# Performance work log

Measured on AMD Instinct MI355X. Metric: run time of the kernel, lower is better.

Reference implementation:

```python
import jax, jax.numpy as jnp
import numpy as np

B, SQ, SK = 2, 2048, 2048
D_MODEL, N_HEADS = 1024, 16
D_HEAD = D_MODEL // N_HEADS
LN_EPS = 1e-5


def _ln(x, w, b):
    # per-head LayerNorm over last dim (d_head)
    mu = jnp.mean(x, axis=-1, keepdims=True)
    var = jnp.mean(jnp.square(x - mu), axis=-1, keepdims=True)
    return (x - mu) * jax.lax.rsqrt(var + LN_EPS) * w + b


def setup_inputs() -> dict:
    key = jax.random.key(0)
    ks = jax.random.split(key, 8)
    sd = 1.0 / np.sqrt(D_MODEL)
    so = 1.0 / np.sqrt(D_HEAD)
    return {
        "x_q": jax.random.normal(ks[0], (B, SQ, D_MODEL), jnp.float32),
        "x_kv": jax.random.normal(ks[1], (B, SK, D_MODEL), jnp.float32),
        "mask": jnp.tril(jnp.ones((SQ, SK), dtype=bool)),  # causal
        "W_Q": jax.random.normal(ks[2], (N_HEADS, D_MODEL, D_HEAD), jnp.float32) * sd,
        "W_K": jax.random.normal(ks[3], (N_HEADS, D_MODEL, D_HEAD), jnp.float32) * sd,
        "W_V": jax.random.normal(ks[4], (N_HEADS, D_MODEL, D_HEAD), jnp.float32) * sd,
        "W_O": jax.random.normal(ks[5], (N_HEADS, D_HEAD, D_MODEL), jnp.float32) * so,
        "b_Q": jnp.zeros((N_HEADS, D_HEAD), jnp.float32),
        "b_K": jnp.zeros((N_HEADS, D_HEAD), jnp.float32),
        "b_V": jnp.zeros((N_HEADS, D_HEAD), jnp.float32),
        "b_O": jnp.zeros((D_MODEL,), jnp.float32),
        "ln1_w": jnp.ones((D_HEAD,), jnp.float32),
        "ln1_b": jnp.zeros((D_HEAD,), jnp.float32),
        "ln2_w": jnp.ones((D_HEAD,), jnp.float32),
        "ln2_b": jnp.zeros((D_HEAD,), jnp.float32),
    }


def reference(x_q, x_kv, mask, W_Q, W_K, W_V, W_O, b_Q, b_K, b_V, b_O,
              ln1_w, ln1_b, ln2_w, ln2_b):
    # QKV projections: b s d, n d h -> b s n h
    q = jnp.einsum('bsd,ndh->bsnh', x_q, W_Q) + b_Q
    k = jnp.einsum('bsd,ndh->bsnh', x_kv, W_K) + b_K
    v = jnp.einsum('bsd,ndh->bsnh', x_kv, W_V) + b_V
    # QK-norm (ln_first=False, rope=None -> just apply LN after projections)
    q = _ln(q, ln1_w, ln1_b)
    k = _ln(k, ln2_w, ln2_b)
    # NOTE: no 1/sqrt(d_head) scaling, matching the original module
    att = jnp.einsum('bqnh,bknh->bnqk', q, k)
    att = jnp.where(mask, att, -jnp.inf)
    probas = jax.nn.softmax(att, axis=-1)
    z = jnp.einsum('bnqk,bknh->bqnh', probas, v)
    out = jnp.einsum('bqnh,nhd->bqd', z, W_O) + b_O
    return (out, k, v)
```

## Files before the change

### kernel.cpp

```cpp
#include <hip/hip_runtime.h>
#include <hip/hip_bf16.h>

#define B_   2
#define SQ_  2048
#define DM_  1024
#define NH_  16
#define DH_  64

typedef __attribute__((ext_vector_type(8))) short          bf16x8;
typedef __attribute__((ext_vector_type(4))) short          bf16x4;
typedef __attribute__((ext_vector_type(8))) unsigned short u16x8;
typedef __attribute__((ext_vector_type(4))) float          f32x4;

__device__ __forceinline__ unsigned short f2bf(float f) {
    union { __hip_bfloat16 h; unsigned short u; } c;
    c.h = __float2bfloat16(f);
    return c.u;
}
__device__ __forceinline__ float gsum16(float v) {
    v += __shfl_xor(v, 1);
    v += __shfl_xor(v, 2);
    v += __shfl_xor(v, 4);
    v += __shfl_xor(v, 8);
    return v;
}

__device__ __forceinline__ f32x4 mfma16(bf16x4 a, bf16x4 b, f32x4 c) {
#if __has_builtin(__builtin_amdgcn_mfma_f32_16x16x16bf16_1k)
    return __builtin_amdgcn_mfma_f32_16x16x16bf16_1k(a, b, c, 0, 0, 0);
#else
    asm("v_mfma_f32_16x16x16_bf16 %0, %1, %2, %0" : "+v"(c) : "v"(a), "v"(b));
    return c;
#endif
}

__device__ __forceinline__ void gll16(const unsigned short* g, unsigned short* l) {
    __builtin_amdgcn_global_load_lds(
        (const __attribute__((address_space(1))) unsigned int*)g,
        (__attribute__((address_space(3))) unsigned int*)l,
        16, 0, 0);
}

__global__ __launch_bounds__(256) void prep_all(
    const float* __restrict__ W_Q, const float* __restrict__ W_K,
    const float* __restrict__ W_V, const float* __restrict__ W_O,
    const float* __restrict__ x_q, const float* __restrict__ x_kv,
    unsigned short* __restrict__ WTq, unsigned short* __restrict__ WTkv,
    unsigned short* __restrict__ WTo,
    unsigned short* __restrict__ xqbf, unsigned short* __restrict__ xkvbf)
{
    const int bid = blockIdx.x, tid = threadIdx.x;
    if (bid >= 1024) {
        const int cid = bid - 1024;
        const float* src = (cid < 512) ? x_q : x_kv;
        unsigned short* dst = (cid < 512) ? xqbf : xkvbf;
        const size_t base = (size_t)(cid & 511) * 8192 + tid * 4;
#pragma unroll
        for (int i = 0; i < 8; ++i) {
            const float4 v = *(const float4*)(src + base + i * 1024);
            ushort4 o;
            o.x = f2bf(v.x); o.y = f2bf(v.y); o.z = f2bf(v.z); o.w = f2bf(v.w);
            *(ushort4*)(dst + base + i * 1024) = o;
        }
        return;
    }
    __shared__ float t[64][65];
    const float* src; unsigned short* dst; int R, C, r0, c0;
    if (bid < 768) {
        const int which = bid >> 8, rem = bid & 255;
        const int rblk = rem & 15, zz = rem >> 4;
        src = (which == 0) ? W_Q : (which == 1) ? W_K : W_V;
        dst = (which == 0) ? WTq : (which == 1) ? WTkv : (WTkv + (1u << 20));
        src += (size_t)65536 * zz;
        dst += (size_t)65536 * zz;
        R = 1024; C = 64; r0 = rblk * 64; c0 = 0;
    } else {
        const int rem = bid - 768;
        src = W_O; dst = WTo; R = 1024; C = 1024;
        r0 = (rem & 15) * 64; c0 = (rem >> 4) * 64;
    }
    const int lr = tid >> 6, lc = tid & 63;
#pragma unroll
    for (int i = 0; i < 16; ++i)
        t[lr + i * 4][lc] = src[(size_t)(r0 + lr + i * 4) * C + c0 + lc];
    __syncthreads();
    const int u = tid & 15, w0 = tid >> 4;
#pragma unroll
    for (int i = 0; i < 4; ++i) {
        const int cl = w0 + i * 16;
        ushort4 o;
        o.x = f2bf(t[4 * u + 0][cl]);
        o.y = f2bf(t[4 * u + 1][cl]);
        o.z = f2bf(t[4 * u + 2][cl]);
        o.w = f2bf(t[4 * u + 3][cl]);
        *(ushort4*)&dst[(size_t)(c0 + cl) * R + r0 + 4 * u] = o;
    }
}

template <int TM, int MODE>
__device__ __forceinline__ void gemm_body(
    unsigned short (*__restrict__ As)[64], unsigned short (*__restrict__ Bs)[64],
    int bx, int by, const unsigned short* __restrict__ Abf,
    const unsigned short* __restrict__ WT,
    const float* __restrict__ biasK, const float* __restrict__ biasV,
    const float* __restrict__ lnw, const float* __restrict__ lnb,
    float* __restrict__ Cf, float* __restrict__ Cf2,
    unsigned short* __restrict__ Cb, unsigned short* __restrict__ CbT, int tid)
{
    constexpr int MI = (TM >= 32) ? TM / 32 : 1;
    constexpr int AJ = TM / 32;

    const int m0 = by * TM;
    const int c0 = bx * 128;

    const int wid = tid >> 6, lane = tid & 63;
    const int wm = (wid >> 1) * (TM / 2);
    const int wn = (wid & 1) * 64;
    const int l15 = lane & 15, qd = lane >> 4;

    const int srow  = tid >> 3;
    const int pslot = tid & 7;
    const int sslot = pslot ^ (srow & 7);
    const unsigned short* Ag = Abf + (size_t)(m0 + (srow % TM)) * 1024 + sslot * 8;
    const unsigned short* Bg = WT  + (size_t)(c0 + srow) * 1024 + sslot * 8;
    unsigned short* Al = &As[srow % TM][pslot * 8];
    unsigned short* Bl = &Bs[srow][pslot * 8];
    const bool athr = (srow < TM);

    const f32x4 zero4 = {0.f, 0.f, 0.f, 0.f};
    f32x4 acc[MI][4];
#pragma unroll
    for (int mi = 0; mi < MI; ++mi)
#pragma unroll
        for (int ni = 0; ni < 4; ++ni) acc[mi][ni] = zero4;

    const int r7 = l15 & 7;

    for (int kb = 0; kb < 16; ++kb) {
        const size_t kof = (size_t)kb * 64;
        __syncthreads();
        if (TM >= 64) {
#pragma unroll
            for (int j = 0; j < AJ; ++j)
                gll16(Ag + (size_t)j * 32 * 1024 + kof, Al + j * 32 * 64);
        } else if (athr) {
            gll16(Ag + kof, Al);
        }
#pragma unroll
        for (int j = 0; j < 4; ++j)
            gll16(Bg + (size_t)j * 32 * 1024 + kof, Bl + j * 32 * 64);
        __syncthreads();
#pragma unroll
        for (int ks = 0; ks < 2; ++ks) {
            const int cs = ((ks * 4 + qd) ^ r7) * 8;
            bf16x8 af[MI], bfr[4];
#pragma unroll
            for (int mi = 0; mi < MI; ++mi)
                af[mi] = *(const bf16x8*)&As[wm + mi * 16 + l15][cs];
#pragma unroll
            for (int ni = 0; ni < 4; ++ni)
                bfr[ni] = *(const bf16x8*)&Bs[wn + ni * 16 + l15][cs];
#pragma unroll
            for (int mi = 0; mi < MI; ++mi)
#pragma unroll
                for (int ni = 0; ni < 4; ++ni)
                    acc[mi][ni] = __builtin_amdgcn_mfma_f32_16x16x32_bf16(
                        af[mi], bfr[ni], acc[mi][ni], 0, 0, 0);
        }
    }

    const float* bias = (MODE == 1 && c0 >= 1024) ? biasV : biasK;
    float bv[4];
#pragma unroll
    for (int ni = 0; ni < 4; ++ni) bv[ni] = bias[(c0 + wn + ni * 16 + l15) & 1023];
#pragma unroll
    for (int mi = 0; mi < MI; ++mi)
#pragma unroll
        for (int ni = 0; ni < 4; ++ni)
#pragma unroll
            for (int r = 0; r < 4; ++r) acc[mi][ni][r] += bv[ni];

    if constexpr (MODE != 2) {
        const bool doLN = (MODE == 0) || (c0 < 1024);
        if (doLN) {
            float w4[4], lb4[4];
#pragma unroll
            for (int ni = 0; ni < 4; ++ni) {
                w4[ni]  = lnw[ni * 16 + l15];
                lb4[ni] = lnb[ni * 16 + l15];
            }
#pragma unroll
            for (int mi = 0; mi < MI; ++mi)
#pragma unroll
                for (int r = 0; r < 4; ++r) {
                    float s1 = acc[mi][0][r] + acc[mi][1][r] + acc[mi][2][r] + acc[mi][3][r];
                    const float mu = gsum16(s1) * (1.0f / 64.0f);
                    float s2 = acc[mi][0][r] * acc[mi][0][r] + acc[mi][1][r] * acc[mi][1][r]
                             + acc[mi][2][r] * acc[mi][2][r] + acc[mi][3][r] * acc[mi][3][r];
                    const float var = gsum16(s2) * (1.0f / 64.0f) - mu * mu;
                    const float rstd = rsqrtf(var + 1e-5f);
#pragma unroll
                    for (int ni = 0; ni < 4; ++ni)
                        acc[mi][ni][r] = (acc[mi][ni][r] - mu) * rstd * w4[ni] + lb4[ni];
                }
        }
    }

    if constexpr (MODE == 0) {
#pragma unroll
        for (int mi = 0; mi < MI; ++mi)
#pragma unroll
            for (int r = 0; r < 4; ++r) {
                const size_t grow = m0 + wm + mi * 16 + qd * 4 + r;
#pragma unroll
                for (int ni = 0; ni < 4; ++ni)
                    Cb[grow * 1024 + c0 + wn + ni * 16 + l15] = f2bf(acc[mi][ni][r]);
            }
    } else if constexpr (MODE == 2) {
#pragma unroll
        for (int mi = 0; mi < MI; ++mi)
#pragma unroll
            for (int r = 0; r < 4; ++r) {
                const size_t grow = m0 + wm + mi * 16 + qd * 4 + r;
#pragma unroll
                for (int ni = 0; ni < 4; ++ni)
                    Cf[grow * 1024 + c0 + wn + ni * 16 + l15] = acc[mi][ni][r];
            }
    } else {
        if (c0 < 1024) {
#pragma unroll
            for (int mi = 0; mi < MI; ++mi)
#pragma unroll
                for (int r = 0; r < 4; ++r) {
                    const size_t grow = m0 + wm + mi * 16 + qd * 4 + r;
#pragma unroll
                    for (int ni = 0; ni < 4; ++ni) {
                        const int gcol = c0 + wn + ni * 16 + l15;
                        Cf[grow * 1024 + gcol] = acc[mi][ni][r];
                        Cb[grow * 1024 + gcol] = f2bf(acc[mi][ni][r]);
                    }
                }
        } else {
#pragma unroll
            for (int mi = 0; mi < MI; ++mi) {
                const int growb = m0 + wm + mi * 16 + qd * 4;
                const int bb_ = growb >> 11, ss = growb & 2047;
#pragma unroll
                for (int ni = 0; ni < 4; ++ni) {
                    const int gv = c0 - 1024 + wn + ni * 16 + l15;
                    const int hh = gv >> 6, dd = gv & 63;
#pragma unroll
                    for (int r = 0; r < 4; ++r)
                        Cf2[(size_t)(growb + r) * 1024 + gv] = acc[mi][ni][r];
                    ushort4 w;
                    w.x = f2bf(acc[mi][ni][0]); w.y = f2bf(acc[mi][ni][1]);
                    w.z = f2bf(acc[mi][ni][2]); w.w = f2bf(acc[mi][ni][3]);
                    *(ushort4*)&CbT[(((size_t)bb_ * NH_ + hh) * DH_ + dd) * SQ_ + ss] = w;
                }
            }
        }
    }
}

__global__ __launch_bounds__(256) void qkv_fused(
    const unsigned short* __restrict__ xqbf, const unsigned short* __restrict__ xkvbf,
    const unsigned short* __restrict__ WTq, const unsigned short* __restrict__ WTkv,
    const float* __restrict__ b_Q, const float* __restrict__ b_K,
    const float* __restrict__ b_V,
    const float* __restrict__ ln1w, const float* __restrict__ ln1b,
    const float* __restrict__ ln2w, const float* __restrict__ ln2b,
    float* __restrict__ kout, float* __restrict__ vout,
    unsigned short* __restrict__ qz, unsigned short* __restrict__ kbf,
    unsigned short* __restrict__ vbfT)
{
    __shared__ __align__(16) unsigned short As[32][64];
    __shared__ __align__(16) unsigned short Bs[128][64];
    const int bid = blockIdx.x, tid = threadIdx.x;
    if (bid < 2048) {
        gemm_body<32, 1>(As, Bs, bid & 15, bid >> 4, xkvbf, WTkv, b_K, b_V,
                         ln2w, ln2b, kout, vout, kbf, vbfT, tid);
    } else {
        const int b2 = bid - 2048;
        gemm_body<32, 0>(As, Bs, b2 & 7, b2 >> 3, xqbf, WTq, b_Q, nullptr,
                         ln1w, ln1b, nullptr, nullptr, qz, nullptr, tid);
    }
}

__global__ __launch_bounds__(256) void o_gemm(
    const unsigned short* __restrict__ zbf, const unsigned short* __restrict__ WTo,
    const float* __restrict__ b_O, float* __restrict__ out)
{
    __shared__ __align__(16) unsigned short As[32][64];
    __shared__ __align__(16) unsigned short Bs[128][64];
    gemm_body<32, 2>(As, Bs, blockIdx.x, blockIdx.y, zbf, WTo, b_O, nullptr,
                     nullptr, nullptr, out, nullptr, nullptr, nullptr, threadIdx.x);
}

__global__ __launch_bounds__(512) void attn_mfma(
    unsigned short* __restrict__ qz, const unsigned short* __restrict__ kbf,
    const unsigned short* __restrict__ vbfT)
{
    __shared__ __align__(16) unsigned short Ks[128][72];
    __shared__ __align__(16) unsigned short VsT[64][136];

    const int tid = threadIdx.x;
    const int h = blockIdx.y, b = blockIdx.z;
    const int wid = tid >> 6, lane = tid & 63;
    const int g = wid & 3, p = wid >> 2;
    const int l15 = lane & 15, qd = lane >> 4;
    const int srow = tid >> 2, scol = (tid & 3) * 16;
    const int vrow = tid >> 3, vcol = (tid & 7) * 16;

    const size_t kbase = (size_t)b * SQ_ * DM_ + (size_t)h * DH_;
    const size_t vbase = ((size_t)b * NH_ + h) * DH_ * (size_t)SQ_;
    const f32x4 zero4 = {0.f, 0.f, 0.f, 0.f};
    const float LOG2E = 1.44269504f, MBIAS = 46.1662413f;

    float* zs = (float*)&Ks[0][0];
    float* ls = (float*)&VsT[0][0];

    for (int pass = 0; pass < 2; ++pass) {
        const int qt = pass ? blockIdx.x : 31 - blockIdx.x;

        bf16x8 qf[2];
        {
            const unsigned short* qp =
                qz + kbase + (size_t)(qt * 64 + g * 16 + l15) * DM_ + qd * 8;
            qf[0] = *(const bf16x8*)(qp);
            qf[1] = *(const bf16x8*)(qp + 32);
        }

        f32x4 z[4];
#pragma unroll
        for (int ni = 0; ni < 4; ++ni) z[ni] = zero4;
        float l_i = 0.f;

        {
            const unsigned short* ks = kbf + kbase + (size_t)srow * DM_ + scol;
            const u16x8 a0 = *(const u16x8*)(ks);
            const u16x8 a1 = *(const u16x8*)(ks + 8);
            const unsigned short* vs = vbfT + vbase + (size_t)vrow * SQ_ + vcol;
            const u16x8 b0 = *(const u16x8*)(vs);
            const u16x8 b1 = *(const u16x8*)(vs + 8);
            *(u16x8*)&Ks[srow][scol + 0]  = a0;
            *(u16x8*)&Ks[srow][scol + 8]  = a1;
            *(u16x8*)&VsT[vrow][vcol + 0] = b0;
            *(u16x8*)&VsT[vrow][vcol + 8] = b1;
        }
        __syncthreads();

        const int NS = (qt >> 1) + 1;
        for (int st = 0; st < NS; ++st) {
            u16x8 kr0, kr1, vr0, vr1;
            if (st < NS - 1) {
                const unsigned short* ks =
                    kbf + kbase + (size_t)((st + 1) * 128 + srow) * DM_ + scol;
                kr0 = *(const u16x8*)(ks);
                kr1 = *(const u16x8*)(ks + 8);
                const unsigned short* vs =
                    vbfT + vbase + (size_t)vrow * SQ_ + (st + 1) * 128 + vcol;
                vr0 = *(const u16x8*)(vs);
                vr1 = *(const u16x8*)(vs + 8);
            }

            const int kt = st * 2 + p;
            if (kt <= qt) {
                f32x4 s[4];
#pragma unroll
                for (int mi = 0; mi < 4; ++mi) s[mi] = zero4;
#pragma unroll
                for (int ks2 = 0; ks2 < 2; ++ks2)
#pragma unroll
                    for (int mi = 0; mi < 4; ++mi) {
                        const bf16x8 af = *(const bf16x8*)
                            &Ks[p * 64 + mi * 16 + l15][ks2 * 32 + qd * 8];
                        s[mi] = __builtin_amdgcn_mfma_f32_16x16x32_bf16(
                            af, qf[ks2], s[mi], 0, 0, 0);
                    }

                if (kt == qt) {
#pragma unroll
                    for (int mi = 0; mi < 4; ++mi)
#pragma unroll
                        for (int r = 0; r < 4; ++r)
                            if (mi * 16 + qd * 4 + r > g * 16 + l15)
                                s[mi][r] = -3.0e38f;
                }

                float ts[4];
                bf16x4 pa[4];
#pragma unroll
                for (int mi = 0; mi < 4; ++mi) {
#pragma unroll
                    for (int r = 0; r < 4; ++r)
                        s[mi][r] = __builtin_amdgcn_exp2f(
                            fmaf(s[mi][r], LOG2E, -MBIAS));
                    ts[mi] = (s[mi][0] + s[mi][1]) + (s[mi][2] + s[mi][3]);
                    pa[mi][0] = (short)f2bf(s[mi][0]);
                    pa[mi][1] = (short)f2bf(s[mi][1]);
                    pa[mi][2] = (short)f2bf(s[mi][2]);
                    pa[mi][3] = (short)f2bf(s[mi][3]);
                }
                float rs = (ts[0] + ts[1]) + (ts[2] + ts[3]);
                rs += __shfl_xor(rs, 16);
                rs += __shfl_xor(rs, 32);
                l_i += rs;

#pragma unroll
                for (int mi = 0; mi < 4; ++mi)
#pragma unroll
                    for (int ni = 0; ni < 4; ++ni) {
                        const bf16x4 bv = *(const bf16x4*)
                            &VsT[ni * 16 + l15][p * 64 + mi * 16 + qd * 4];
                        z[ni] = mfma16(pa[mi], bv, z[ni]);
                    }
            }
            __syncthreads();
            if (st < NS - 1) {
                *(u16x8*)&Ks[srow][scol + 0]  = kr0;
                *(u16x8*)&Ks[srow][scol + 8]  = kr1;
                *(u16x8*)&VsT[vrow][vcol + 0] = vr0;
                *(u16x8*)&VsT[vrow][vcol + 8] = vr1;
            }
            __syncthreads();
        }

        if (p == 1) {
#pragma unroll
            for (int ni = 0; ni < 4; ++ni)
                *(f32x4*)&zs[((g * 4 + ni) * 64 + lane) * 4] = z[ni];
            ls[g * 64 + lane] = l_i;
        }
        __syncthreads();
        if (p == 0) {
            const float l_tot = l_i + ls[g * 64 + lane];
#pragma unroll
            for (int ni = 0; ni < 4; ++ni) {
                const f32x4 zo = *(const f32x4*)&zs[((g * 4 + ni) * 64 + lane) * 4];
#pragma unroll
                for (int r = 0; r < 4; ++r) z[ni][r] += zo[r];
            }
            const float linv = 1.0f / l_tot;
#pragma unroll
            for (int r = 0; r < 4; ++r) {
                const float lr_ = __shfl(linv, qd * 4 + r);
                const size_t row = (size_t)qt * 64 + g * 16 + qd * 4 + r;
#pragma unroll
                for (int ni = 0; ni < 4; ++ni)
                    qz[kbase + row * DM_ + ni * 16 + l15] = f2bf(z[ni][r] * lr_);
            }
        }
        __syncthreads();
    }
}

extern "C" void kernel_launch(void* const* d_in, const int* in_sizes, int n_in,
                              void* d_out, int out_size, void* d_ws, size_t ws_size,
                              hipStream_t stream)
{
    const float* x_q  = (const float*)d_in[0];
    const float* x_kv = (const float*)d_in[1];
    const float* W_Q  = (const float*)d_in[3];
    const float* W_K  = (const float*)d_in[4];
    const float* W_V  = (const float*)d_in[5];
    const float* W_O  = (const float*)d_in[6];
    const float* b_Q  = (const float*)d_in[7];
    const float* b_K  = (const float*)d_in[8];
    const float* b_V  = (const float*)d_in[9];
    const float* b_O  = (const float*)d_in[10];
    const float* ln1w = (const float*)d_in[11];
    const float* ln1b = (const float*)d_in[12];
    const float* ln2w = (const float*)d_in[13];
    const float* ln2b = (const float*)d_in[14];

    const size_t NTOK = (size_t)B_ * SQ_;
    float* out  = (float*)d_out;
    float* kout = out + NTOK * DM_;
    float* vout = kout + NTOK * DM_;

    unsigned short* xqbf  = (unsigned short*)out;
    unsigned short* xkvbf = xqbf + (1u << 22);

    unsigned short* wsu  = (unsigned short*)d_ws;
    unsigned short* WTq  = wsu;
    unsigned short* WTkv = WTq + (1u << 20);
    unsigned short* WTo  = WTkv + (2u << 20);
    unsigned short* qz   = WTo + (1u << 20);
    unsigned short* kbf  = qz + (1u << 22);
    unsigned short* vbfT = kbf + (1u << 22);

    prep_all<<<2048, 256, 0, stream>>>(W_Q, W_K, W_V, W_O, x_q, x_kv,
                                       WTq, WTkv, WTo, xqbf, xkvbf);

    qkv_fused<<<3072, 256, 0, stream>>>(xqbf, xkvbf, WTq, WTkv, b_Q, b_K, b_V,
                                        ln1w, ln1b, ln2w, ln2b,
                                        kout, vout, qz, kbf, vbfT);

    attn_mfma<<<dim3(16, NH_, B_), 512, 0, stream>>>(qz, kbf, vbfT);

    o_gemm<<<dim3(8, 128), 256, 0, stream>>>(qz, WTo, b_O, out);
}
```

Before: 236.4 us.

## Enlarge QKV GEMM tile to 128x128 with 512-thread blocks

Generalizes the GEMM body over thread count and row-tile size, then switches the fused QKV projection from 32x128 tiles with 256 threads to 128x128 tiles with 512 threads. Each B (weight) tile loaded into shared memory is now reused across four times as many rows, which cuts global/L2 traffic for weights and the number of blocks. The cost is fewer blocks (768) and more LDS per block, which may lower occupancy and latency hiding.

Measured after the change: 228.8 us. 1.03x faster.

```diff
diff --git a/kernel.cpp b/kernel.cpp
--- a/kernel.cpp
+++ b/kernel.cpp
@@ -97,7 +97,7 @@
     }
 }
 
-template <int TM, int MODE>
+template <int TM, int MODE, int NT>
 __device__ __forceinline__ void gemm_body(
     unsigned short (*__restrict__ As)[64], unsigned short (*__restrict__ Bs)[64],
     int bx, int by, const unsigned short* __restrict__ Abf,
@@ -107,25 +107,28 @@
     float* __restrict__ Cf, float* __restrict__ Cf2,
     unsigned short* __restrict__ Cb, unsigned short* __restrict__ CbT, int tid)
 {
-    constexpr int MI = (TM >= 32) ? TM / 32 : 1;
-    constexpr int AJ = TM / 32;
+    constexpr int NW    = NT / 64;
+    constexpr int WROWS = 2 * TM / NW;
+    constexpr int MI    = WROWS / 16;
+    constexpr int RP    = NT / 8;
+    constexpr int APASS = TM / RP;
+    constexpr int BPASS = 128 / RP;
 
     const int m0 = by * TM;
     const int c0 = bx * 128;
 
     const int wid = tid >> 6, lane = tid & 63;
-    const int wm = (wid >> 1) * (TM / 2);
+    const int wm = (wid >> 1) * WROWS;
     const int wn = (wid & 1) * 64;
     const int l15 = lane & 15, qd = lane >> 4;
 
     const int srow  = tid >> 3;
     const int pslot = tid & 7;
     const int sslot = pslot ^ (srow & 7);
-    const unsigned short* Ag = Abf + (size_t)(m0 + (srow % TM)) * 1024 + sslot * 8;
+    const unsigned short* Ag = Abf + (size_t)(m0 + srow) * 1024 + sslot * 8;
     const unsigned short* Bg = WT  + (size_t)(c0 + srow) * 1024 + sslot * 8;
-    unsigned short* Al = &As[srow % TM][pslot * 8];
+    unsigned short* Al = &As[srow][pslot * 8];
     unsigned short* Bl = &Bs[srow][pslot * 8];
-    const bool athr = (srow < TM);
 
     const f32x4 zero4 = {0.f, 0.f, 0.f, 0.f};
     f32x4 acc[MI][4];
@@ -139,16 +142,12 @@
     for (int kb = 0; kb < 16; ++kb) {
         const size_t kof = (size_t)kb * 64;
         __syncthreads();
-        if (TM >= 64) {
-#pragma unroll
-            for (int j = 0; j < AJ; ++j)
-                gll16(Ag + (size_t)j * 32 * 1024 + kof, Al + j * 32 * 64);
-        } else if (athr) {
-            gll16(Ag + kof, Al);
-        }
-#pragma unroll
-        for (int j = 0; j < 4; ++j)
-            gll16(Bg + (size_t)j * 32 * 1024 + kof, Bl + j * 32 * 64);
+#pragma unroll
+        for (int j = 0; j < APASS; ++j)
+            gll16(Ag + (size_t)j * RP * 1024 + kof, Al + j * RP * 64);
+#pragma unroll
+        for (int j = 0; j < BPASS; ++j)
+            gll16(Bg + (size_t)j * RP * 1024 + kof, Bl + j * RP * 64);
         __syncthreads();
 #pragma unroll
         for (int ks = 0; ks < 2; ++ks) {
@@ -262,7 +261,7 @@
     }
 }
 
-__global__ __launch_bounds__(256) void qkv_fused(
+__global__ __launch_bounds__(512) void qkv_fused(
     const unsigned short* __restrict__ xqbf, const unsigned short* __restrict__ xkvbf,
     const unsigned short* __restrict__ WTq, const unsigned short* __restrict__ WTkv,
     const float* __restrict__ b_Q, const float* __restrict__ b_K,
@@ -273,16 +272,16 @@
     unsigned short* __restrict__ qz, unsigned short* __restrict__ kbf,
     unsigned short* __restrict__ vbfT)
 {
-    __shared__ __align__(16) unsigned short As[32][64];
+    __shared__ __align__(16) unsigned short As[128][64];
     __shared__ __align__(16) unsigned short Bs[128][64];
     const int bid = blockIdx.x, tid = threadIdx.x;
-    if (bid < 2048) {
-        gemm_body<32, 1>(As, Bs, bid & 15, bid >> 4, xkvbf, WTkv, b_K, b_V,
-                         ln2w, ln2b, kout, vout, kbf, vbfT, tid);
+    if (bid < 512) {
+        gemm_body<128, 1, 512>(As, Bs, bid & 15, bid >> 4, xkvbf, WTkv, b_K, b_V,
+                               ln2w, ln2b, kout, vout, kbf, vbfT, tid);
     } else {
-        const int b2 = bid - 2048;
-        gemm_body<32, 0>(As, Bs, b2 & 7, b2 >> 3, xqbf, WTq, b_Q, nullptr,
-                         ln1w, ln1b, nullptr, nullptr, qz, nullptr, tid);
+        const int b2 = bid - 512;
+        gemm_body<128, 0, 512>(As, Bs, b2 & 7, b2 >> 3, xqbf, WTq, b_Q, nullptr,
+                               ln1w, ln1b, nullptr, nullptr, qz, nullptr, tid);
     }
 }
 
@@ -292,8 +291,8 @@
 {
     __shared__ __align__(16) unsigned short As[32][64];
     __shared__ __align__(16) unsigned short Bs[128][64];
-    gemm_body<32, 2>(As, Bs, blockIdx.x, blockIdx.y, zbf, WTo, b_O, nullptr,
-                     nullptr, nullptr, out, nullptr, nullptr, nullptr, threadIdx.x);
+    gemm_body<32, 2, 256>(As, Bs, blockIdx.x, blockIdx.y, zbf, WTo, b_O, nullptr,
+                          nullptr, nullptr, out, nullptr, nullptr, nullptr, threadIdx.x);
 }
 
 __global__ __launch_bounds__(512) void attn_mfma(
@@ -492,9 +491,9 @@
     prep_all<<<2048, 256, 0, stream>>>(W_Q, W_K, W_V, W_O, x_q, x_kv,
                                        WTq, WTkv, WTo, xqbf, xkvbf);
 
-    qkv_fused<<<3072, 256, 0, stream>>>(xqbf, xkvbf, WTq, WTkv, b_Q, b_K, b_V,
-                                        ln1w, ln1b, ln2w, ln2b,
-                                        kout, vout, qz, kbf, vbfT);
+    qkv_fused<<<768, 512, 0, stream>>>(xqbf, xkvbf, WTq, WTkv, b_Q, b_K, b_V,
+                                       ln1w, ln1b, ln2w, ln2b,
+                                       kout, vout, qz, kbf, vbfT);
 
     attn_mfma<<<dim3(16, NH_, B_), 512, 0, stream>>>(qz, kbf, vbfT);
 
```
